# Kernel optimization log

Hardware: AMD Instinct MI355X
Metric: run time of the kernel (lower is better)

Reference implementation:

```python
import jax, jax.numpy as jnp
import numpy as np

SAMPLES = 16        # samples per spatial dim -> M = SAMPLES**2 sample points
SAMPLE_PAD = 0
K = 9               # nearest neighbors == conv kernel size == stride


def setup_inputs() -> dict:
    key = jax.random.key(0)
    k1, k2, k3 = jax.random.split(key, 3)
    B, C, H, W = 16, 128, 64, 64
    OUT = 128
    x = jax.random.normal(k1, (B, C, H, W), dtype=jnp.float32)
    w = jax.random.normal(k2, (OUT, C, K), dtype=jnp.float32) * 0.05
    b = jax.random.normal(k3, (OUT,), dtype=jnp.float32) * 0.05
    return {"x": x, "w": w, "b": b}


def reference(x, w, b):
    B, C, H, W = x.shape
    N = H * W
    # --- spatial sample grid (static, shape-derived) ---
    xi = jnp.round(jnp.linspace(SAMPLE_PAD, H - SAMPLE_PAD - 1, SAMPLES)).astype(jnp.int32)
    yi = jnp.round(jnp.linspace(SAMPLE_PAD, W - SAMPLE_PAD - 1, SAMPLES)).astype(jnp.int32)
    xg, yg = jnp.meshgrid(xi, yi, indexing='ij')
    x_sample = x[:, :, xg, yg].reshape(B, C, -1)          # (B, C, M)
    x1 = x.reshape(B, C, N)                                # (B, C, N)
    # --- squared Euclidean distance between tokens and samples ---
    dots = jnp.einsum('bcn,bcm->bnm', x1, x_sample)        # (B, N, M)
    n2 = jnp.sum(x1 * x1, axis=1)                          # (B, N)
    m2 = jnp.sum(x_sample * x_sample, axis=1)              # (B, M)
    dist2 = n2[:, :, None] + m2[:, None, :] - 2.0 * dots   # (B, N, M)
    # K nearest samples per token (smallest distance)
    _, idx = jax.lax.top_k(-dist2, K)                      # (B, N, K) int32
    # gather neighbor features from the sample set: (B, C, N, K)
    nbrs = jnp.take_along_axis(x_sample[:, :, None, :],
                               idx[:, None, :, :], axis=3)
    # Conv1d(kernel=K, stride=K) over the (B, C, N*K) prime tensor
    out = jnp.einsum('bcnk,ock->bon', nbrs, w) + b[None, :, None]
    return out.reshape(B, w.shape[0], H, W)
```

## Files before the change

### kernel.cpp

```cpp
#include <hip/hip_runtime.h>

#define NB   16
#define NC   128
#define NN   4096
#define NM   256
#define NK   9
#define NO   128

__device__ __constant__ int d_grid16[16] = {0,4,8,13,17,21,25,29,34,38,42,46,50,55,59,63};

__global__ __launch_bounds__(256) void k_wr(const float* __restrict__ w,
                                            float* __restrict__ Wr) {
    int f = blockIdx.x * 256 + threadIdx.x;
    int o = f & 127;
    int k = (f >> 7) % 9;
    int c = f / 1152;
    Wr[f] = w[o * 1152 + c * 9 + k];
}

__global__ __launch_bounds__(256) void k_gather(const float* __restrict__ x,
                                                float* __restrict__ xs) {
    int bc = blockIdx.x;
    int m  = threadIdx.x;
    int pix = d_grid16[m >> 4] * 64 + d_grid16[m & 15];
    xs[bc * NM + m] = x[bc * NN + pix];
}

__global__ __launch_bounds__(256) void k_m2(const float* __restrict__ xs,
                                            float* __restrict__ m2) {
    #pragma clang fp contract(off)
    int f = blockIdx.x * 256 + threadIdx.x;
    int b = f >> 8, m = f & 255;
    const float* p = xs + (size_t)b * NC * NM + m;
    float a = 0.f;
    #pragma unroll 4
    for (int c = 0; c < NC; ++c) { float v = p[c * NM]; a = __fadd_rn(a, __fmul_rn(v, v)); }
    m2[f] = a;
}

__global__ __launch_bounds__(256) void k_n2(const float* __restrict__ x,
                                            float* __restrict__ n2) {
    #pragma clang fp contract(off)
    int f = blockIdx.x * 256 + threadIdx.x;
    int b = f >> 12, n = f & 4095;
    const float* p = x + (size_t)b * NC * NN + n;
    float a = 0.f;
    #pragma unroll 4
    for (int c = 0; c < NC; ++c) { float v = p[(size_t)c * NN]; a = __fadd_rn(a, __fmul_rn(v, v)); }
    n2[f] = a;
}

__global__ __launch_bounds__(256) void k_g(const float* __restrict__ xs,
                                           const float* __restrict__ Wr,
                                           float* __restrict__ G) {
    __shared__ float xsl[64 * 64];
    __shared__ float wl[64 * 128];
    int kk = blockIdx.x, mt = blockIdx.y, b = blockIdx.z;
    int t = threadIdx.x;
    int to = t & 31, tmm = t >> 5;
    float acc[8][4] = {};
    for (int c0 = 0; c0 < NC; c0 += 64) {
        __syncthreads();
        #pragma unroll
        for (int it = 0; it < 16; ++it) {
            int f = it * 256 + t;
            int cc = f >> 6, mm = f & 63;
            xsl[f] = xs[((size_t)b * NC + c0 + cc) * NM + mt * 64 + mm];
        }
        #pragma unroll
        for (int it = 0; it < 32; ++it) {
            int f = it * 256 + t;
            int cc = f >> 7, o = f & 127;
            wl[f] = Wr[(size_t)(c0 + cc) * 1152 + kk * 128 + o];
        }
        __syncthreads();
        for (int cc = 0; cc < 64; ++cc) {
            const float4 a0 = *(const float4*)&xsl[cc * 64 + tmm * 8];
            const float4 a1 = *(const float4*)&xsl[cc * 64 + tmm * 8 + 4];
            float av[8] = {a0.x, a0.y, a0.z, a0.w, a1.x, a1.y, a1.z, a1.w};
            float2 w0 = *(const float2*)&wl[cc * 128 + 2 * to];
            float2 w1 = *(const float2*)&wl[cc * 128 + 64 + 2 * to];
            float wv[4] = {w0.x, w0.y, w1.x, w1.y};
            #pragma unroll
            for (int i = 0; i < 8; ++i)
                #pragma unroll
                for (int j = 0; j < 4; ++j)
                    acc[i][j] = fmaf(av[i], wv[j], acc[i][j]);
        }
    }
    #pragma unroll
    for (int i = 0; i < 8; ++i) {
        size_t base = (((size_t)(b * NM + mt * 64 + tmm * 8 + i) * NK + kk) << 7);
        *(float2*)&G[base + 2 * to]      = make_float2(acc[i][0], acc[i][1]);
        *(float2*)&G[base + 64 + 2 * to] = make_float2(acc[i][2], acc[i][3]);
    }
}

__device__ inline unsigned long long shfl_xor_u64(unsigned long long v, int m) {
    int lo = __shfl_xor((int)(v & 0xFFFFFFFFull), m, 64);
    int hi = __shfl_xor((int)(v >> 32), m, 64);
    return ((unsigned long long)(unsigned)hi << 32) | (unsigned)lo;
}

__global__ __launch_bounds__(256) void k_sel(const float* __restrict__ x,
                                             const float* __restrict__ xs,
                                             const float* __restrict__ n2,
                                             const float* __restrict__ m2,
                                             int* __restrict__ idx) {
    #pragma clang fp contract(off)
    __shared__ float sm[9216];
    __shared__ float m2l[256];
    __shared__ float n2l[32];
    int b = blockIdx.y, n0 = blockIdx.x * 32;
    int t = threadIdx.x;
    int tm = t & 31, tn = t >> 5;
    m2l[t] = m2[b * NM + t];
    if (t < 32) n2l[t] = n2[b * NN + n0 + t];
    float acc[4][8];
    #pragma unroll
    for (int i = 0; i < 4; ++i)
        #pragma unroll
        for (int j = 0; j < 8; ++j) acc[i][j] = 0.f;

    for (int c0 = 0; c0 < NC; c0 += 32) {
        __syncthreads();
        #pragma unroll
        for (int it = 0; it < 4; ++it) {
            int f = it * 256 + t;
            int cc = f >> 5, nn = f & 31;
            sm[f] = x[((size_t)b * NC + c0 + cc) * NN + n0 + nn];
        }
        #pragma unroll
        for (int it = 0; it < 32; ++it) {
            int f = it * 256 + t;
            int cc = f >> 8, m = f & 255;
            sm[1024 + f] = xs[((size_t)b * NC + c0 + cc) * NM + m];
        }
        __syncthreads();
        for (int cc = 0; cc < 32; ++cc) {
            const float4 a4 = *(const float4*)&sm[cc * 32 + tn * 4];
            float av[4] = {a4.x, a4.y, a4.z, a4.w};
            float2 s0 = *(const float2*)&sm[1024 + cc * 256 + 2 * tm];
            float2 s1 = *(const float2*)&sm[1024 + cc * 256 + 64 + 2 * tm];
            float2 s2 = *(const float2*)&sm[1024 + cc * 256 + 128 + 2 * tm];
            float2 s3 = *(const float2*)&sm[1024 + cc * 256 + 192 + 2 * tm];
            float sv[8] = {s0.x, s0.y, s1.x, s1.y, s2.x, s2.y, s3.x, s3.y};
            #pragma unroll
            for (int i = 0; i < 4; ++i)
                #pragma unroll
                for (int j = 0; j < 8; ++j)
                    acc[i][j] = __fadd_rn(acc[i][j], __fmul_rn(av[i], sv[j]));
        }
    }
    __syncthreads();
    unsigned* keysl = (unsigned*)sm;
    int   mj[8];
    float m2v[8];
    #pragma unroll
    for (int j = 0; j < 8; ++j) { mj[j] = (j >> 1) * 64 + 2 * tm + (j & 1); m2v[j] = m2l[mj[j]]; }
    #pragma unroll
    for (int i = 0; i < 4; ++i) {
        int n = tn * 4 + i;
        float n2v = n2l[n];
        #pragma unroll
        for (int j = 0; j < 8; ++j) {
            float key = __fsub_rn(__fadd_rn(n2v, m2v[j]), __fmul_rn(2.f, acc[i][j]));
            unsigned u = __float_as_uint(key);
            u ^= (u & 0x80000000u) ? 0xFFFFFFFFu : 0x80000000u;
            keysl[n * 258 + mj[j]] = u;
        }
    }
    __syncthreads();
    {
        int n = t >> 3, q = t & 7;
        unsigned long long bk[9];
        #pragma unroll
        for (int j = 0; j < 9; ++j) bk[j] = ~0ull;
        for (int i = 0; i < 32; ++i) {
            int m = q + 8 * i;
            unsigned long long v = ((unsigned long long)keysl[n * 258 + m] << 32) | (unsigned)m;
            if (v < bk[8]) {
                #pragma unroll
                for (int j = 0; j < 9; ++j) {
                    unsigned long long t0 = bk[j];
                    bool c = v < t0;
                    bk[j] = c ? v : t0;
                    v     = c ? t0 : v;
                }
            }
        }
        #pragma unroll
        for (int rr = 1; rr <= 4; rr <<= 1) {
            unsigned long long pv[9];
            #pragma unroll
            for (int j = 0; j < 9; ++j) pv[j] = shfl_xor_u64(bk[j], rr);
            #pragma unroll
            for (int j = 0; j < 9; ++j) {
                unsigned long long v = pv[j];
                if (v >= bk[8]) break;
                #pragma unroll
                for (int jj = 0; jj < 9; ++jj) {
                    unsigned long long t0 = bk[jj];
                    bool c = v < t0;
                    bk[jj] = c ? v : t0;
                    v      = c ? t0 : v;
                }
            }
        }
        if (q == 0) {
            size_t base = (size_t)(b * NN + n0 + n) * NK;
            #pragma unroll
            for (int k = 0; k < 9; ++k) idx[base + k] = (int)(unsigned)(bk[k] & 0xFFFFFFFFull);
        }
    }
}

__global__ __launch_bounds__(256) void k_out(const float* __restrict__ G,
                                             const int* __restrict__ idx,
                                             const float* __restrict__ bias,
                                             float* __restrict__ out) {
    __shared__ float S[64 * 129];
    __shared__ int   idxl[576];
    __shared__ float biasl[128];
    int b = blockIdx.y, n0 = blockIdx.x * 64;
    int t = threadIdx.x;
    if (t < 128) biasl[t] = bias[t];
    for (int f = t; f < 576; f += 256) idxl[f] = idx[(size_t)(b * NN + n0) * NK + f];
    __syncthreads();
    int o = t & 127, half = t >> 7;
    for (int p = 0; p < 32; ++p) {
        int n = p * 2 + half;
        float a = biasl[o];
        #pragma unroll
        for (int k = 0; k < 9; ++k) {
            int m = idxl[n * 9 + k];
            a += G[(((size_t)(b * NM + m)) * NK + k) * 128 + o];
        }
        S[n * 129 + o] = a;
    }
    __syncthreads();
    int nn = t & 63, ob = t >> 6;
    for (int p = 0; p < 32; ++p) {
        int o2 = p * 4 + ob;
        out[((size_t)(b * NO + o2)) * NN + n0 + nn] = S[nn * 129 + o2];
    }
}

extern "C" void kernel_launch(void* const* d_in, const int* in_sizes, int n_in,
                              void* d_out, int out_size, void* d_ws, size_t ws_size,
                              hipStream_t stream) {
    const float* x    = (const float*)d_in[0];
    const float* w    = (const float*)d_in[1];
    const float* bias = (const float*)d_in[2];
    float* out = (float*)d_out;

    float* ws  = (float*)d_ws;
    float* n2  = ws;
    float* m2  = ws + 65536;
    float* xs  = ws + 69632;
    float* Wr  = ws + 593920;
    float* G   = ws + 741376;
    int*   idx = (int*)(ws + 5459968);

    k_wr    <<<dim3(576),       dim3(256), 0, stream>>>(w, Wr);
    k_gather<<<dim3(2048),      dim3(256), 0, stream>>>(x, xs);
    k_m2    <<<dim3(16),        dim3(256), 0, stream>>>(xs, m2);
    k_n2    <<<dim3(256),       dim3(256), 0, stream>>>(x, n2);
    k_g     <<<dim3(9, 4, 16),  dim3(256), 0, stream>>>(xs, Wr, G);
    k_sel   <<<dim3(128, 16),   dim3(256), 0, stream>>>(x, xs, n2, m2, idx);
    k_out   <<<dim3(64, 16),    dim3(256), 0, stream>>>(G, idx, bias, out);
}
```

Baseline: 272.6 us.

## Split KNN selection into fast FMA candidate filter plus exact refinement pass

The selection kernel now computes distances with fused multiply-add, drops the per-token norm term (constant per row), and emits up to 16 candidate samples within a small margin of the 9th-best score. A new refinement kernel recomputes exact, contraction-off distances only for those candidates and ranks them, which preserves the reference's tie and rounding behaviour. The separate n2 kernel is removed, and the tile loads are vectorised to float4. This removes the strict non-contracted arithmetic from the dense distance GEMM, at the cost of an extra kernel that re-reads x and xs. It also risks wrong results if more than 16 candidates fall inside the margin.

New measurement: 294.6 us. 1.08x slower.

```diff
diff --git a/kernel.cpp b/kernel.cpp
--- a/kernel.cpp
+++ b/kernel.cpp
@@ -6,6 +6,8 @@
 #define NM   256
 #define NK   9
 #define NO   128
+
+#define DELTA 0.0078125f
 
 __device__ __constant__ int d_grid16[16] = {0,4,8,13,17,21,25,29,34,38,42,46,50,55,59,63};
 
@@ -36,18 +38,6 @@
     #pragma unroll 4
     for (int c = 0; c < NC; ++c) { float v = p[c * NM]; a = __fadd_rn(a, __fmul_rn(v, v)); }
     m2[f] = a;
-}
-
-__global__ __launch_bounds__(256) void k_n2(const float* __restrict__ x,
-                                            float* __restrict__ n2) {
-    #pragma clang fp contract(off)
-    int f = blockIdx.x * 256 + threadIdx.x;
-    int b = f >> 12, n = f & 4095;
-    const float* p = x + (size_t)b * NC * NN + n;
-    float a = 0.f;
-    #pragma unroll 4
-    for (int c = 0; c < NC; ++c) { float v = p[(size_t)c * NN]; a = __fadd_rn(a, __fmul_rn(v, v)); }
-    n2[f] = a;
 }
 
 __global__ __launch_bounds__(256) void k_g(const float* __restrict__ xs,
@@ -104,18 +94,16 @@
 
 __global__ __launch_bounds__(256) void k_sel(const float* __restrict__ x,
                                              const float* __restrict__ xs,
-                                             const float* __restrict__ n2,
                                              const float* __restrict__ m2,
-                                             int* __restrict__ idx) {
-    #pragma clang fp contract(off)
+                                             unsigned short* __restrict__ cand) {
     __shared__ float sm[9216];
     __shared__ float m2l[256];
-    __shared__ float n2l[32];
+    __shared__ int   cntl[32];
     int b = blockIdx.y, n0 = blockIdx.x * 32;
     int t = threadIdx.x;
     int tm = t & 31, tn = t >> 5;
     m2l[t] = m2[b * NM + t];
-    if (t < 32) n2l[t] = n2[b * NN + n0 + t];
+    if (t < 32) cntl[t] = 0;
     float acc[4][8];
     #pragma unroll
     for (int i = 0; i < 4; ++i)
@@ -124,17 +112,17 @@
 
     for (int c0 = 0; c0 < NC; c0 += 32) {
         __syncthreads();
-        #pragma unroll
-        for (int it = 0; it < 4; ++it) {
-            int f = it * 256 + t;
-            int cc = f >> 5, nn = f & 31;
-            sm[f] = x[((size_t)b * NC + c0 + cc) * NN + n0 + nn];
-        }
-        #pragma unroll
-        for (int it = 0; it < 32; ++it) {
-            int f = it * 256 + t;
-            int cc = f >> 8, m = f & 255;
-            sm[1024 + f] = xs[((size_t)b * NC + c0 + cc) * NM + m];
+        {
+            int cc = t >> 3, nn4 = (t & 7) * 4;
+            *(float4*)&sm[cc * 32 + nn4] =
+                *(const float4*)&x[((size_t)b * NC + c0 + cc) * NN + n0 + nn4];
+        }
+        #pragma unroll
+        for (int it = 0; it < 8; ++it) {
+            int f4 = it * 256 + t;
+            int cc = f4 >> 6, mm4 = (f4 & 63) * 4;
+            *(float4*)&sm[1024 + cc * 256 + mm4] =
+                *(const float4*)&xs[((size_t)b * NC + c0 + cc) * NM + mm4];
         }
         __syncthreads();
         for (int cc = 0; cc < 32; ++cc) {
@@ -149,11 +137,10 @@
             for (int i = 0; i < 4; ++i)
                 #pragma unroll
                 for (int j = 0; j < 8; ++j)
-                    acc[i][j] = __fadd_rn(acc[i][j], __fmul_rn(av[i], sv[j]));
-        }
-    }
-    __syncthreads();
-    unsigned* keysl = (unsigned*)sm;
+                    acc[i][j] = fmaf(av[i], sv[j], acc[i][j]);
+        }
+    }
+    __syncthreads();
     int   mj[8];
     float m2v[8];
     #pragma unroll
@@ -161,14 +148,9 @@
     #pragma unroll
     for (int i = 0; i < 4; ++i) {
         int n = tn * 4 + i;
-        float n2v = n2l[n];
-        #pragma unroll
-        for (int j = 0; j < 8; ++j) {
-            float key = __fsub_rn(__fadd_rn(n2v, m2v[j]), __fmul_rn(2.f, acc[i][j]));
-            unsigned u = __float_as_uint(key);
-            u ^= (u & 0x80000000u) ? 0xFFFFFFFFu : 0x80000000u;
-            keysl[n * 258 + mj[j]] = u;
-        }
+        #pragma unroll
+        for (int j = 0; j < 8; ++j)
+            sm[n * 258 + mj[j]] = fmaf(-2.f, acc[i][j], m2v[j]);
     }
     __syncthreads();
     {
@@ -178,7 +160,9 @@
         for (int j = 0; j < 9; ++j) bk[j] = ~0ull;
         for (int i = 0; i < 32; ++i) {
             int m = q + 8 * i;
-            unsigned long long v = ((unsigned long long)keysl[n * 258 + m] << 32) | (unsigned)m;
+            unsigned u = __float_as_uint(sm[n * 258 + m]);
+            u = (u & 0x80000000u) ? ~u : (u | 0x80000000u);
+            unsigned long long v = ((unsigned long long)u << 32) | (unsigned)m;
             if (v < bk[8]) {
                 #pragma unroll
                 for (int j = 0; j < 9; ++j) {
@@ -207,11 +191,96 @@
                 }
             }
         }
+        unsigned u9 = (unsigned)(bk[8] >> 32);
+        u9 = (u9 & 0x80000000u) ? (u9 & 0x7FFFFFFFu) : ~u9;
+        float theta = __uint_as_float(u9) + DELTA;
+        size_t tokbase = (size_t)(b * NN + n0 + n) * 16;
+        for (int i = 0; i < 32; ++i) {
+            int m = q + 8 * i;
+            if (sm[n * 258 + m] <= theta) {
+                int pos = atomicAdd(&cntl[n], 1);
+                if (pos < 16) cand[tokbase + pos] = (unsigned short)m;
+            }
+        }
+        __syncthreads();
         if (q == 0) {
-            size_t base = (size_t)(b * NN + n0 + n) * NK;
-            #pragma unroll
-            for (int k = 0; k < 9; ++k) idx[base + k] = (int)(unsigned)(bk[k] & 0xFFFFFFFFull);
-        }
+            int c = cntl[n]; if (c > 16) c = 16;
+            for (int s = c; s < 16; ++s) cand[tokbase + s] = 0xFFFFu;
+        }
+    }
+}
+
+__global__ __launch_bounds__(256) void k_ref(const float* __restrict__ x,
+                                             const float* __restrict__ xs,
+                                             const float* __restrict__ m2,
+                                             const unsigned short* __restrict__ cand,
+                                             int* __restrict__ idx) {
+    #pragma clang fp contract(off)
+    __shared__ float xsl[32 * 256];
+    __shared__ float x1l[32 * 32];
+    __shared__ float m2l[256];
+    __shared__ unsigned long long pairs[32 * 16];
+    int b = blockIdx.y, n0 = blockIdx.x * 32;
+    int t = threadIdx.x;
+    m2l[t] = m2[b * NM + t];
+    int r = t >> 3, q = t & 7;
+    int n = n0 + r;
+    size_t tokbase = (size_t)(b * NN + n) * 16;
+    int mA = cand[tokbase + q];
+    int mB = cand[tokbase + 8 + q];
+    bool vA = (mA != 0xFFFF), vB = (mB != 0xFFFF);
+    int mAx = vA ? mA : 0, mBx = vB ? mB : 0;
+    float dotA = 0.f, dotB = 0.f, n2 = 0.f;
+    for (int c0 = 0; c0 < NC; c0 += 32) {
+        __syncthreads();
+        {
+            int cc = t >> 3, nn4 = (t & 7) * 4;
+            *(float4*)&x1l[cc * 32 + nn4] =
+                *(const float4*)&x[((size_t)b * NC + c0 + cc) * NN + n0 + nn4];
+        }
+        #pragma unroll
+        for (int it = 0; it < 8; ++it) {
+            int f4 = it * 256 + t;
+            int cc = f4 >> 6, mm4 = (f4 & 63) * 4;
+            *(float4*)&xsl[cc * 256 + mm4] =
+                *(const float4*)&xs[((size_t)b * NC + c0 + cc) * NM + mm4];
+        }
+        __syncthreads();
+        for (int cc = 0; cc < 32; ++cc) {
+            float xv = x1l[cc * 32 + r];
+            n2   = __fadd_rn(n2,   __fmul_rn(xv, xv));
+            dotA = __fadd_rn(dotA, __fmul_rn(xv, xsl[cc * 256 + mAx]));
+            dotB = __fadd_rn(dotB, __fmul_rn(xv, xsl[cc * 256 + mBx]));
+        }
+    }
+    unsigned long long pA = ~0ull, pB = ~0ull;
+    if (vA) {
+        float key = __fsub_rn(__fadd_rn(n2, m2l[mAx]), __fmul_rn(2.f, dotA));
+        unsigned u = __float_as_uint(key);
+        u = (u & 0x80000000u) ? ~u : (u | 0x80000000u);
+        pA = ((unsigned long long)u << 32) | (unsigned)mAx;
+    }
+    if (vB) {
+        float key = __fsub_rn(__fadd_rn(n2, m2l[mBx]), __fmul_rn(2.f, dotB));
+        unsigned u = __float_as_uint(key);
+        u = (u & 0x80000000u) ? ~u : (u | 0x80000000u);
+        pB = ((unsigned long long)u << 32) | (unsigned)mBx;
+    }
+    pairs[r * 16 + q]     = pA;
+    pairs[r * 16 + 8 + q] = pB;
+    __syncthreads();
+    size_t obase = (size_t)(b * NN + n) * NK;
+    if (vA) {
+        int rank = 0;
+        #pragma unroll
+        for (int j = 0; j < 16; ++j) rank += (pairs[r * 16 + j] < pA);
+        if (rank < 9) idx[obase + rank] = mAx;
+    }
+    if (vB) {
+        int rank = 0;
+        #pragma unroll
+        for (int j = 0; j < 16; ++j) rank += (pairs[r * 16 + j] < pB);
+        if (rank < 9) idx[obase + rank] = mBx;
     }
 }
 
@@ -255,18 +324,18 @@
     float* out = (float*)d_out;
 
     float* ws  = (float*)d_ws;
-    float* n2  = ws;
-    float* m2  = ws + 65536;
-    float* xs  = ws + 69632;
-    float* Wr  = ws + 593920;
-    float* G   = ws + 741376;
-    int*   idx = (int*)(ws + 5459968);
+    float* m2  = ws;
+    float* xs  = ws + 4096;
+    float* Wr  = ws + 528384;
+    float* G   = ws + 675840;
+    int*   idx = (int*)(ws + 5394432);
+    unsigned short* cand = (unsigned short*)(ws + 5984256);
 
     k_wr    <<<dim3(576),       dim3(256), 0, stream>>>(w, Wr);
     k_gather<<<dim3(2048),      dim3(256), 0, stream>>>(x, xs);
     k_m2    <<<dim3(16),        dim3(256), 0, stream>>>(xs, m2);
-    k_n2    <<<dim3(256),       dim3(256), 0, stream>>>(x, n2);
     k_g     <<<dim3(9, 4, 16),  dim3(256), 0, stream>>>(xs, Wr, G);
-    k_sel   <<<dim3(128, 16),   dim3(256), 0, stream>>>(x, xs, n2, m2, idx);
+    k_sel   <<<dim3(128, 16),   dim3(256), 0, stream>>>(x, xs, m2, cand);
+    k_ref   <<<dim3(128, 16),   dim3(256), 0, stream>>>(x, xs, m2, cand, idx);
     k_out   <<<dim3(64, 16),    dim3(256), 0, stream>>>(G, idx, bias, out);
 }
```
